# Kernel tuning notes

Hardware: AMD Instinct MI355X
Metric: run time of the kernel (lower is better)

The kernel has to match this reference:

```python
import jax, jax.numpy as jnp
import numpy as np

N = 40000      # nodes
E = 640000     # directed edges (avg degree 16)
IN_DIM = 64
HID = 64
OUT = 128
EPS_LN = 1e-5
EPS_BN = 1e-5
NEG_SLOPE = 0.2  # PyG GATConv default


def setup_inputs() -> dict:
    key = jax.random.key(0)
    ks = jax.random.split(key, 40)
    s = 0.05
    d = {}
    d["x"] = jax.random.normal(ks[0], (N, IN_DIM), jnp.float32)
    d["edge_index"] = jax.random.randint(ks[1], (2, E), 0, N, jnp.int32)
    d["pos"] = jax.random.normal(ks[2], (N, 3), jnp.float32)
    # GAT layer 1: in=64, out=64, heads=4 (concat)
    d["W1"] = jax.random.normal(ks[3], (4 * HID, IN_DIM), jnp.float32) * s
    d["a_s1"] = jax.random.normal(ks[4], (4, HID), jnp.float32) * s
    d["a_d1"] = jax.random.normal(ks[5], (4, HID), jnp.float32) * s
    d["bg1"] = jnp.zeros((4 * HID,), jnp.float32)
    d["ln1_g"] = jnp.ones((4 * HID,), jnp.float32)
    d["ln1_b"] = jnp.zeros((4 * HID,), jnp.float32)
    # GAT layer 2: in=256, out=64, heads=2 (concat)
    d["W2"] = jax.random.normal(ks[6], (2 * HID, 4 * HID), jnp.float32) * s
    d["a_s2"] = jax.random.normal(ks[7], (2, HID), jnp.float32) * s
    d["a_d2"] = jax.random.normal(ks[8], (2, HID), jnp.float32) * s
    d["bg2"] = jnp.zeros((2 * HID,), jnp.float32)
    d["ln2_g"] = jnp.ones((2 * HID,), jnp.float32)
    d["ln2_b"] = jnp.zeros((2 * HID,), jnp.float32)
    # GAT layer 3: in=128, out=128, heads=1
    d["W3"] = jax.random.normal(ks[9], (OUT, 2 * HID), jnp.float32) * s
    d["a_s3"] = jax.random.normal(ks[10], (1, OUT), jnp.float32) * s
    d["a_d3"] = jax.random.normal(ks[11], (1, OUT), jnp.float32) * s
    d["bg3"] = jnp.zeros((OUT,), jnp.float32)
    # pointnet: Conv1d(3,64,1) -> BN -> ReLU -> Conv1d(64,128,1) -> BN -> ReLU -> Conv1d(128,128,1)
    d["pw1"] = jax.random.normal(ks[12], (64, 3), jnp.float32) * s
    d["pb1"] = jnp.zeros((64,), jnp.float32)
    d["bn1_g"] = jnp.ones((64,), jnp.float32)
    d["bn1_b"] = jnp.zeros((64,), jnp.float32)
    d["pw2"] = jax.random.normal(ks[13], (128, 64), jnp.float32) * s
    d["pb2"] = jnp.zeros((128,), jnp.float32)
    d["bn2_g"] = jnp.ones((128,), jnp.float32)
    d["bn2_b"] = jnp.zeros((128,), jnp.float32)
    d["pw3"] = jax.random.normal(ks[14], (OUT, 128), jnp.float32) * s
    d["pb3"] = jnp.zeros((OUT,), jnp.float32)
    # fusion Linear(2*OUT, OUT)
    d["fw"] = jax.random.normal(ks[15], (OUT, 2 * OUT), jnp.float32) * s
    d["fb"] = jnp.zeros((OUT,), jnp.float32)
    return d


def _gat(x, W, a_s, a_d, b, src, dst, n):
    """PyG-style GATConv (concat=True, eval mode). x:[n,Fin], W:[H*C,Fin], a_*:[H,C]."""
    H, C = a_s.shape
    h = (x @ W.T).reshape(n, H, C)                       # [n,H,C]
    e_src = jnp.sum(h * a_s[None], -1)                   # [n,H]
    e_dst = jnp.sum(h * a_d[None], -1)                   # [n,H]
    e = jax.nn.leaky_relu(e_src[src] + e_dst[dst], NEG_SLOPE)   # [E,H]
    emax = jax.ops.segment_max(e, dst, num_segments=n)   # segment softmax over dst
    ex = jnp.exp(e - emax[dst])
    den = jax.ops.segment_sum(ex, dst, num_segments=n)
    alpha = ex / (den[dst] + 1e-16)                      # [E,H]
    out = jax.ops.segment_sum(alpha[:, :, None] * h[src], dst, num_segments=n)  # [n,H,C]
    return out.reshape(n, H * C) + b


def _ln(x, g, b):
    mu = jnp.mean(x, -1, keepdims=True)
    var = jnp.var(x, -1, keepdims=True)
    return (x - mu) * jax.lax.rsqrt(var + EPS_LN) * g + b


def _bn_eval(x, g, b):
    # eval-mode BatchNorm with freshly-initialized running stats (mean=0, var=1)
    return x * (g * jax.lax.rsqrt(jnp.float32(1.0 + EPS_BN))) + b


def reference(x, edge_index, pos, W1, a_s1, a_d1, bg1, ln1_g, ln1_b,
              W2, a_s2, a_d2, bg2, ln2_g, ln2_b, W3, a_s3, a_d3, bg3,
              pw1, pb1, bn1_g, bn1_b, pw2, pb2, bn2_g, bn2_b, pw3, pb3, fw, fb):
    n = x.shape[0]
    loops = jnp.arange(n, dtype=edge_index.dtype)        # PyG add_self_loops=True
    src = jnp.concatenate([edge_index[0], loops])
    dst = jnp.concatenate([edge_index[1], loops])

    x1 = jax.nn.relu(_ln(_gat(x, W1, a_s1, a_d1, bg1, src, dst, n), ln1_g, ln1_b))
    x2 = jax.nn.relu(_ln(_gat(x1, W2, a_s2, a_d2, bg2, src, dst, n), ln2_g, ln2_b))
    x3 = _gat(x2, W3, a_s3, a_d3, bg3, src, dst, n)      # [n,OUT]

    # pointnet: 1x1 conv1d == per-node linear
    p = jax.nn.relu(_bn_eval(pos @ pw1.T + pb1, bn1_g, bn1_b))
    p = jax.nn.relu(_bn_eval(p @ pw2.T + pb2, bn2_g, bn2_b))
    pos_features = p @ pw3.T + pb3                       # [n,OUT]

    combined = jnp.concatenate([x3, pos_features], -1)
    output = combined @ fw.T + fb
    return (output, x3, pos_features)
```

## Files before the change

kernel.cpp:

```cpp
#include <hip/hip_runtime.h>
#include <cstddef>

#define NNODES 40000
#define NEDGES 640000
#define NETOT  (NNODES + NEDGES)
#define ELLW   96
#define NCAST  30720
#define NBUCK  313
#define SEGCAP 8192
#define ABLOCKS 84
#define CBLOCKS 30
#define GBLK   625

typedef unsigned short u16;
typedef unsigned int   u32;
using v2f = __attribute__((ext_vector_type(2))) float;

__device__ inline float wave_sum(float v) {
#pragma unroll
    for (int o = 32; o > 0; o >>= 1) v += __shfl_xor(v, o);
    return v;
}
__device__ inline u16 f2bf(float f) {
    u32 u = __float_as_uint(f);
    return (u16)((u + 0x7fffu + ((u >> 16) & 1u)) >> 16);
}

__global__ void build_a_kernel(const int* __restrict__ ei, u32* __restrict__ bcnt,
                               u32* __restrict__ seg,
                               const float* __restrict__ W1, const float* __restrict__ as1,
                               const float* __restrict__ ad1, float* __restrict__ vbuf,
                               const float* s0, u16* d0, int n0, const float* s1, u16* d1, int n1,
                               const float* s2, u16* d2, int n2, const float* s3, u16* d3, int n3,
                               const float* s4, u16* d4, int n4, const float* s5, u16* d5, int n5) {
    int tid = threadIdx.x;
    int blk = blockIdx.x;
    if (blk >= ABLOCKS) {
        if (blk < ABLOCKS + CBLOCKS) {
            int i = (blk - ABLOCKS) * 1024 + tid;
            const float* s; u16* d;
            if      (i < n0) { s = s0; d = d0; }
            else if ((i -= n0) < n1) { s = s1; d = d1; }
            else if ((i -= n1) < n2) { s = s2; d = d2; }
            else if ((i -= n2) < n3) { s = s3; d = d3; }
            else if ((i -= n3) < n4) { s = s4; d = d4; }
            else if ((i -= n4) < n5) { s = s5; d = d5; }
            else return;
            float4 v = ((const float4*)s)[i];
            ushort4 o; o.x = f2bf(v.x); o.y = f2bf(v.y); o.z = f2bf(v.z); o.w = f2bf(v.w);
            ((ushort4*)d)[i] = o;
        } else if (tid < 256) {
            int h = tid >> 6, k = tid & 63;
            float ss = 0.f, dd = 0.f;
            for (int c = 0; c < 64; c++) {
                float w = W1[(h * 64 + c) * 64 + k];
                ss += as1[h * 64 + c] * w;
                dd += ad1[h * 64 + c] * w;
            }
            vbuf[tid] = ss;
            vbuf[256 + tid] = dd;
        }
        return;
    }
    __shared__ u32 hist[NBUCK], hbase[NBUCK];
    for (int i = tid; i < NBUCK; i += 1024) hist[i] = 0;
    __syncthreads();
    u32 pk[8], loc[8]; int bj[8];
    int g0 = blk * 8192;
#pragma unroll
    for (int j = 0; j < 8; j++) {
        int g = g0 + j * 1024 + tid;
        bj[j] = -1;
        if (g < NETOT) {
            int src, dst;
            if (g < NEDGES) { src = ei[g]; dst = ei[NEDGES + g]; }
            else            { src = g - NEDGES; dst = src; }
            int b = dst >> 7;
            pk[j] = ((u32)dst << 16) | (u32)src;
            bj[j] = b;
            loc[j] = atomicAdd(&hist[b], 1u);
        }
    }
    __syncthreads();
    for (int i = tid; i < NBUCK; i += 1024) {
        u32 c = hist[i];
        hbase[i] = c ? atomicAdd(&bcnt[i], c) : 0u;
    }
    __syncthreads();
#pragma unroll
    for (int j = 0; j < 8; j++) {
        if (bj[j] >= 0) {
            u32 pos = hbase[bj[j]] + loc[j];
            if (pos < SEGCAP) seg[(size_t)bj[j] * SEGCAP + pos] = pk[j];
        }
    }
}

__global__ void mid_kernel(const u32* __restrict__ seg, const u32* __restrict__ bcnt,
                           int* __restrict__ cnt, u16* __restrict__ srcs16,
                           int2* __restrict__ ovbuf,
                           const float* __restrict__ x, const float* __restrict__ vbuf,
                           float* __restrict__ es, float* __restrict__ ed, u16* __restrict__ xc,
                           const float* __restrict__ pos,
                           const float* __restrict__ pw1, const float* __restrict__ pb1,
                           const float* __restrict__ bn1g, const float* __restrict__ bn1b,
                           const u16* __restrict__ Bpn, u16* __restrict__ p2out,
                           const float* __restrict__ pb2,
                           const float* __restrict__ bn2g, const float* __restrict__ bn2b) {
    __shared__ u32 lcnt[128];
    __shared__ float vl[512];
    int tid = threadIdx.x;
    int blk = blockIdx.x;

    if (blk < NBUCK) {
        int base = blk << 7;
        if (tid < 128) lcnt[tid] = 0;
        __syncthreads();
        u32 m = bcnt[blk]; if (m > SEGCAP) m = SEGCAP;
        const u32* sp = seg + (size_t)blk * SEGCAP;
        for (u32 e = tid; e < m; e += 256) {
            u32 pkv = sp[e];
            u32 dst = pkv >> 16, src = pkv & 0xffffu;
            u32 p = atomicAdd(&lcnt[dst - (u32)base], 1u);
            if (p < ELLW) srcs16[dst * ELLW + p] = (u16)src;
            else {
                int q = atomicAdd(&cnt[NNODES], 1);
                ovbuf[q] = make_int2((int)dst, (int)src);
            }
        }
        __syncthreads();
        if (tid < 128 && base + tid < NNODES) cnt[base + tid] = (int)lcnt[tid];
        return;
    }
    blk -= NBUCK;
    if (blk < GBLK) {
        vl[tid] = vbuf[tid];
        vl[tid + 256] = vbuf[tid + 256];
        __syncthreads();
        int lane = tid & 63, wave = tid >> 6;
        int i = lane >> 2, q = lane & 3;
        int node = blk * 64 + wave * 16 + i;
        const float* xp = x + (size_t)node * 64 + q * 16;
        float xr[16];
        *(float4*)&xr[0]  = ((const float4*)xp)[0];
        *(float4*)&xr[4]  = ((const float4*)xp)[1];
        *(float4*)&xr[8]  = ((const float4*)xp)[2];
        *(float4*)&xr[12] = ((const float4*)xp)[3];
        float p[8];
#pragma unroll
        for (int h = 0; h < 8; h++) {
            float s = 0.f;
#pragma unroll
            for (int j = 0; j < 16; j++) s += xr[j] * vl[h * 64 + q * 16 + j];
            p[h] = s;
        }
#pragma unroll
        for (int h = 0; h < 8; h++) {
            p[h] += __shfl_xor(p[h], 1);
            p[h] += __shfl_xor(p[h], 2);
        }
        es[node * 4 + q] = p[q];
        ed[node * 4 + q] = p[4 + q];
        u16* cp = xc + (size_t)node * 64 + q * 16;
#pragma unroll
        for (int j = 0; j < 16; j += 4) {
            ushort4 o; o.x = f2bf(xr[j]); o.y = f2bf(xr[j + 1]);
            o.z = f2bf(xr[j + 2]); o.w = f2bf(xr[j + 3]);
            *(ushort4*)(cp + j) = o;
        }
        return;
    }
    blk -= GBLK;
    {
        const int Nn = 128, K = 64;
        using bfrag = __attribute__((ext_vector_type(8))) short;
        using ffrag = __attribute__((ext_vector_type(4))) float;
        int wave = tid >> 6, lane = tid & 63;
        int lm = lane & 15, kg = (lane >> 4) * 8;
        int rowblk = blk * 64 + wave * 16;
        int row = rowblk + lm;
        float p0 = pos[row * 3 + 0], p1 = pos[row * 3 + 1], p2 = pos[row * 3 + 2];
        const u16* Bp = Bpn + (size_t)lm * K + kg;
        const float bnscale = rsqrtf(1.0f + 1e-5f);
        ffrag acc[8] = {};
#pragma unroll
        for (int k0 = 0; k0 < K; k0 += 32) {
            bfrag af;
#pragma unroll
            for (int j = 0; j < 8; j++) {
                int k = kg + k0 + j;
                float v = p0 * pw1[k * 3 + 0] + p1 * pw1[k * 3 + 1] + p2 * pw1[k * 3 + 2] + pb1[k];
                v = v * (bn1g[k] * bnscale) + bn1b[k];
                v = v > 0.f ? v : 0.f;
                af[j] = (short)f2bf(v);
            }
#pragma unroll
            for (int t = 0; t < 8; t++) {
                bfrag bf = *(const bfrag*)(Bp + (size_t)t * 16 * K + k0);
                acc[t] = __builtin_amdgcn_mfma_f32_16x16x32_bf16(af, bf, acc[t], 0, 0, 0);
            }
        }
        int orow = rowblk + (lane >> 4) * 4;
#pragma unroll
        for (int t = 0; t < 8; t++) {
            int col = t * 16 + lm;
            float bi = pb2[col], g = bn2g[col] * bnscale, bb = bn2b[col];
#pragma unroll
            for (int r = 0; r < 4; r++) {
                float v = (acc[t][r] + bi) * g + bb;
                v = v > 0.f ? v : 0.f;
                p2out[(size_t)(orow + r) * Nn + col] = f2bf(v);
            }
        }
    }
}

__global__ void gat_agg_kernel(const u16* __restrict__ xc,
                               const float* __restrict__ es, const float* __restrict__ ed,
                               const int* __restrict__ cnt, const u16* __restrict__ srcs16,
                               const int2* __restrict__ ovbuf,
                               u16* __restrict__ agg, int n) {
    __shared__ float wbuf[4][4][100];
    __shared__ u32   sbuf[4][ELLW];
    int wave = threadIdx.x >> 6;
    int wid = (blockIdx.x * blockDim.x + threadIdx.x) >> 6;
    int lane = threadIdx.x & 63;
    if (wid >= n) return;

    int degt = cnt[wid];
    int mainc = degt < ELLW ? degt : ELLW;
    int padt = (mainc + 7) & ~7;
    const u16* sp = srcs16 + (size_t)wid * ELLW;

    const int h = lane & 3;
    const int esub = lane >> 2;
    float edh = ed[(size_t)wid * 4 + h];

    float den = 0.f;
    for (int i0 = 0; i0 < padt; i0 += 16) {
        int e = i0 + esub;
        if (e < padt) {
            float w = 0.f; u32 off = 0;
            if (e < mainc) {
                int s = sp[e];
                off = (u32)s << 7;
                float v = es[(size_t)s * 4 + h] + edh;
                v = v > 0.f ? v : 0.2f * v;
                w = __expf(v);
            }
            wbuf[wave][h][e] = w;
            if (h == 0) sbuf[wave][e] = off;
            den += w;
        }
    }
    int ovn = 0;
    if (degt > ELLW) {
        ovn = cnt[n];
        for (int j = esub; j < ovn; j += 16) {
            int2 t = ovbuf[j];
            if (t.x == wid) {
                float v = es[(size_t)t.y * 4 + h] + edh;
                v = v > 0.f ? v : 0.2f * v;
                den += __expf(v);
            }
        }
    }
#pragma unroll
    for (int o = 4; o < 64; o <<= 1) den += __shfl_xor(den, o);
    float inv = 1.f / (den + 1e-16f);

    const int e2 = lane >> 5, f16 = lane & 31;
    const char* hp = (const char*)xc + f16 * 4;
    v2f a0 = {0.f, 0.f}, a1 = {0.f, 0.f}, a2 = {0.f, 0.f}, a3 = {0.f, 0.f};
    for (int eb = 0; eb < padt; eb += 8) {
        u32 of[4]; u32 g[4];
        float w0[4], w1[4], w2[4], w3[4];
#pragma unroll
        for (int k = 0; k < 4; k++) of[k] = sbuf[wave][eb + 2 * k + e2];
#pragma unroll
        for (int k = 0; k < 4; k++) g[k] = *(const u32*)(hp + of[k]);
#pragma unroll
        for (int k = 0; k < 4; k++) {
            int e = eb + 2 * k + e2;
            w0[k] = wbuf[wave][0][e]; w1[k] = wbuf[wave][1][e];
            w2[k] = wbuf[wave][2][e]; w3[k] = wbuf[wave][3][e];
        }
#pragma unroll
        for (int k = 0; k < 4; k++) {
            v2f hx;
            hx.x = __uint_as_float(g[k] << 16);
            hx.y = __uint_as_float(g[k] & 0xffff0000u);
            a0 += v2f{w0[k], w0[k]} * hx;
            a1 += v2f{w1[k], w1[k]} * hx;
            a2 += v2f{w2[k], w2[k]} * hx;
            a3 += v2f{w3[k], w3[k]} * hx;
        }
    }
    if (degt > ELLW) {
        for (int j = 0; j < ovn; j++) {
            int2 t = ovbuf[j];
            if (t.x != wid) continue;
            float wh[4];
#pragma unroll
            for (int hh = 0; hh < 4; hh++) {
                float v = es[(size_t)t.y * 4 + hh] + __shfl(edh, hh);
                v = v > 0.f ? v : 0.2f * v;
                wh[hh] = __expf(v);
            }
            if (lane < 32) {
                u32 g = *(const u32*)(hp + ((u32)t.y << 7));
                v2f hx;
                hx.x = __uint_as_float(g << 16);
                hx.y = __uint_as_float(g & 0xffff0000u);
                a0 += v2f{wh[0], wh[0]} * hx;
                a1 += v2f{wh[1], wh[1]} * hx;
                a2 += v2f{wh[2], wh[2]} * hx;
                a3 += v2f{wh[3], wh[3]} * hx;
            }
        }
    }
    a0.x += __shfl_xor(a0.x, 32); a0.y += __shfl_xor(a0.y, 32);
    a1.x += __shfl_xor(a1.x, 32); a1.y += __shfl_xor(a1.y, 32);
    a2.x += __shfl_xor(a2.x, 32); a2.y += __shfl_xor(a2.y, 32);
    a3.x += __shfl_xor(a3.x, 32); a3.y += __shfl_xor(a3.y, 32);
    float iv[4];
#pragma unroll
    for (int hh = 0; hh < 4; hh++) iv[hh] = __shfl(inv, hh);
    if (lane < 32) {
        u32* op = (u32*)agg + (size_t)wid * 128 + f16;
        op[0]  = ((u32)f2bf(a0.y * iv[0]) << 16) | f2bf(a0.x * iv[0]);
        op[32] = ((u32)f2bf(a1.y * iv[1]) << 16) | f2bf(a1.x * iv[1]);
        op[64] = ((u32)f2bf(a2.y * iv[2]) << 16) | f2bf(a2.x * iv[2]);
        op[96] = ((u32)f2bf(a3.y * iv[3]) << 16) | f2bf(a3.x * iv[3]);
    }
}

__global__ __launch_bounds__(256, 2) void w1ln_kernel(
                            const u16* __restrict__ agg, const u16* __restrict__ B,
                            const float* __restrict__ bias,
                            const float* __restrict__ lng, const float* __restrict__ lnb,
                            u16* __restrict__ xb, int M) {
    using bfrag = __attribute__((ext_vector_type(8))) short;
    using ffrag = __attribute__((ext_vector_type(4))) float;
    int wave = threadIdx.x >> 6, lane = threadIdx.x & 63;
    int lm = lane & 15, kg = (lane >> 4) * 8;
    int rowblk = blockIdx.x * 64 + wave * 16;
    ffrag acc[16] = {};
#pragma unroll
    for (int hh = 0; hh < 4; hh++) {
#pragma unroll
        for (int k0 = 0; k0 < 64; k0 += 32) {
            bfrag af = *(const bfrag*)(agg + (size_t)(rowblk + lm) * 256 + hh * 64 + kg + k0);
            bfrag bfs[4];
#pragma unroll
            for (int tt = 0; tt < 4; tt++)
                bfs[tt] = *(const bfrag*)(B + (size_t)(hh * 64 + tt * 16 + lm) * 64 + kg + k0);
#pragma unroll
            for (int tt = 0; tt < 4; tt++) {
                int t = hh * 4 + tt;
                acc[t] = __builtin_amdgcn_mfma_f32_16x16x32_bf16(af, bfs[tt], acc[t], 0, 0, 0);
            }
        }
    }
    int orow = rowblk + (lane >> 4) * 4;
    float bi[16], gg[16], bb[16];
#pragma unroll
    for (int t = 0; t < 16; t++) {
        int col = t * 16 + lm;
        bi[t] = bias[col]; gg[t] = lng[col]; bb[t] = lnb[col];
    }
#pragma unroll
    for (int r = 0; r < 4; r++) {
        float pv[16];
        float s1 = 0.f, s2 = 0.f;
#pragma unroll
        for (int t = 0; t < 16; t++) {
            float v = acc[t][r] + bi[t];
            pv[t] = v; s1 += v; s2 += v * v;
        }
#pragma unroll
        for (int o = 1; o < 16; o <<= 1) { s1 += __shfl_xor(s1, o); s2 += __shfl_xor(s2, o); }
        float mu = s1 / 256.f;
        float var = s2 / 256.f - mu * mu;
        float rstd = rsqrtf(var + 1e-5f);
#pragma unroll
        for (int t = 0; t < 16; t++) {
            float v = (pv[t] - mu) * rstd * gg[t] + bb[t];
            v = v > 0.f ? v : 0.f;
            xb[(size_t)(orow + r) * 256 + t * 16 + lm] = f2bf(v);
        }
    }
}

template <int H, int C, bool AF32>
__global__ __launch_bounds__(256, 2) void gemm_scores_kernel(
                                   const void* __restrict__ Aptr, const u16* __restrict__ B,
                                   u16* __restrict__ Cout,
                                   const float* __restrict__ as, const float* __restrict__ ad,
                                   float* __restrict__ es, float* __restrict__ ed,
                                   int M, int Nn, int K) {
    constexpr int HT = 128 / C;
    using bfrag = __attribute__((ext_vector_type(8))) short;
    using ffrag = __attribute__((ext_vector_type(4))) float;
    int wave = threadIdx.x >> 6, lane = threadIdx.x & 63;
    int lm = lane & 15, kg = (lane >> 4) * 8;
    int rowblk = blockIdx.x * 64 + wave * 16;
    int n0 = blockIdx.y * 128;
    const u16* Bp = B + (size_t)(n0 + lm) * K + kg;
    ffrag acc[8] = {};
    for (int k0 = 0; k0 < K; k0 += 32) {
        bfrag af;
        if constexpr (AF32) {
            const float* ap = (const float*)Aptr + (size_t)(rowblk + lm) * K + kg + k0;
            float4 a0 = *(const float4*)ap;
            float4 a1 = *(const float4*)(ap + 4);
            af[0] = (short)f2bf(a0.x); af[1] = (short)f2bf(a0.y);
            af[2] = (short)f2bf(a0.z); af[3] = (short)f2bf(a0.w);
            af[4] = (short)f2bf(a1.x); af[5] = (short)f2bf(a1.y);
            af[6] = (short)f2bf(a1.z); af[7] = (short)f2bf(a1.w);
        } else {
            af = *(const bfrag*)((const u16*)Aptr + (size_t)(rowblk + lm) * K + kg + k0);
        }
        bfrag bfs[8];
#pragma unroll
        for (int t = 0; t < 8; t++)
            bfs[t] = *(const bfrag*)(Bp + (size_t)t * 16 * K + k0);
#pragma unroll
        for (int t = 0; t < 8; t++)
            acc[t] = __builtin_amdgcn_mfma_f32_16x16x32_bf16(af, bfs[t], acc[t], 0, 0, 0);
    }
    int orow = rowblk + (lane >> 4) * 4;
    float asv[8], adv[8];
#pragma unroll
    for (int t = 0; t < 8; t++) {
        int fcol = n0 + t * 16 + lm;
        asv[t] = as[fcol]; adv[t] = ad[fcol];
    }
    float ps[4][HT] = {}, pd[4][HT] = {};
#pragma unroll
    for (int t = 0; t < 8; t++) {
        const int hh = t / (C / 16);
#pragma unroll
        for (int r = 0; r < 4; r++) {
            float v = acc[t][r];
            ps[r][hh] += v * asv[t];
            pd[r][hh] += v * adv[t];
            Cout[(size_t)(orow + r) * Nn + n0 + t * 16 + lm] = f2bf(v);
        }
    }
    int hb = blockIdx.y * HT;
#pragma unroll
    for (int r = 0; r < 4; r++)
#pragma unroll
        for (int hh = 0; hh < HT; hh++) {
            float s = ps[r][hh], d = pd[r][hh];
#pragma unroll
            for (int o = 1; o < 16; o <<= 1) { s += __shfl_xor(s, o); d += __shfl_xor(d, o); }
            if (lm == 0) {
                es[(size_t)(orow + r) * H + hb + hh] = s;
                ed[(size_t)(orow + r) * H + hb + hh] = d;
            }
        }
}

template <int H, int C, bool LNRELU>
__global__ void gat_fused_kernel(const u16* __restrict__ hmat,
                                 const float* __restrict__ es, const float* __restrict__ ed,
                                 const int* __restrict__ cnt, const u16* __restrict__ srcs16,
                                 const int2* __restrict__ ovbuf,
                                 const float* __restrict__ bias,
                                 const float* __restrict__ lng, const float* __restrict__ lnb,
                                 void* __restrict__ out, u16* __restrict__ x16out, int n) {
    constexpr int HC = H * C;
    constexpr int VPT = HC / 64;
    constexpr int SH = (HC == 256) ? 9 : 8;
    constexpr int EPW = 64 / H;
    constexpr int HSH = (H == 4) ? 2 : ((H == 2) ? 1 : 0);
    __shared__ float wbuf[4][H][100];
    __shared__ int   sbuf[4][ELLW];
    int wave = threadIdx.x >> 6;
    int wid = (blockIdx.x * blockDim.x + threadIdx.x) >> 6;
    int lane = threadIdx.x & 63;
    if (wid >= n) return;

    int degt = cnt[wid];
    int mainc = degt < ELLW ? degt : ELLW;
    int pad = (mainc + 7) & ~7;
    const u16* sp = srcs16 + (size_t)wid * ELLW;

    const int h = lane & (H - 1);
    const int esub = lane >> HSH;
    float edh = ed[(size_t)wid * H + h];

    float den = 0.f;
    for (int i0 = 0; i0 < pad; i0 += EPW) {
        int e = i0 + esub;
        if (e < pad) {
            float w = 0.f;
            int soff = 0;
            if (e < mainc) {
                int s = sp[e];
                soff = s << SH;
                float v = es[(size_t)s * H + h] + edh;
                v = v > 0.f ? v : 0.2f * v;
                w = __expf(v);
            }
            wbuf[wave][h][e] = w;
            if (h == 0) sbuf[wave][e] = soff;
            den += w;
        }
    }
    int ovn = 0;
    if (degt > ELLW) {
        ovn = cnt[n];
        for (int j = esub; j < ovn; j += EPW) {
            int2 t = ovbuf[j];
            if (t.x == wid) {
                float v = es[(size_t)t.y * H + h] + edh;
                v = v > 0.f ? v : 0.2f * v;
                den += __expf(v);
            }
        }
    }
#pragma unroll
    for (int o = H; o < 64; o <<= 1) den += __shfl_xor(den, o);
    float inv = 1.f / (den + 1e-16f);

    const int myhead = (lane * VPT) / C;
    const float invh = __shfl(inv, myhead);
    const int loff = lane * (VPT * 2);
    v2f a01 = {0.f, 0.f}, a23 = {0.f, 0.f};

    for (int e = 0; e < pad; e += 8) {
        int4   o0 = *(const int4*)&sbuf[wave][e];
        int4   o1 = *(const int4*)&sbuf[wave][e + 4];
        float4 w0 = *(const float4*)&wbuf[wave][myhead][e];
        float4 w1 = *(const float4*)&wbuf[wave][myhead][e + 4];
        int   oo[8] = {o0.x, o0.y, o0.z, o0.w, o1.x, o1.y, o1.z, o1.w};
        float ww[8] = {w0.x, w0.y, w0.z, w0.w, w1.x, w1.y, w1.z, w1.w};
        if constexpr (VPT == 4) {
            uint2 gg[8];
#pragma unroll
            for (int u = 0; u < 8; u++)
                gg[u] = *(const uint2*)((const char*)hmat + (size_t)(u32)oo[u] + loff);
#pragma unroll
            for (int u = 0; u < 8; u++) {
                v2f wv = {ww[u], ww[u]};
                v2f h01, h23;
                h01.x = __uint_as_float(gg[u].x << 16);
                h01.y = __uint_as_float(gg[u].x & 0xffff0000u);
                h23.x = __uint_as_float(gg[u].y << 16);
                h23.y = __uint_as_float(gg[u].y & 0xffff0000u);
                a01 += wv * h01;
                a23 += wv * h23;
            }
        } else {
            u32 gg[8];
#pragma unroll
            for (int u = 0; u < 8; u++)
                gg[u] = *(const u32*)((const char*)hmat + (size_t)(u32)oo[u] + loff);
#pragma unroll
            for (int u = 0; u < 8; u++) {
                v2f wv = {ww[u], ww[u]};
                v2f h01;
                h01.x = __uint_as_float(gg[u] << 16);
                h01.y = __uint_as_float(gg[u] & 0xffff0000u);
                a01 += wv * h01;
            }
        }
    }
    if (degt > ELLW) {
        const float edm = __shfl(edh, myhead);
        for (int j = 0; j < ovn; j++) {
            int2 t = ovbuf[j];
            if (t.x != wid) continue;
            float v = es[(size_t)t.y * H + myhead] + edm;
            v = v > 0.f ? v : 0.2f * v;
            float w = __expf(v);
            v2f wv = {w, w};
            if constexpr (VPT == 4) {
                uint2 g = *(const uint2*)((const char*)hmat + ((size_t)t.y << SH) + loff);
                v2f h01, h23;
                h01.x = __uint_as_float(g.x << 16);
                h01.y = __uint_as_float(g.x & 0xffff0000u);
                h23.x = __uint_as_float(g.y << 16);
                h23.y = __uint_as_float(g.y & 0xffff0000u);
                a01 += wv * h01;
                a23 += wv * h23;
            } else {
                u32 g = *(const u32*)((const char*)hmat + ((size_t)t.y << SH) + loff);
                v2f h01;
                h01.x = __uint_as_float(g << 16);
                h01.y = __uint_as_float(g & 0xffff0000u);
                a01 += wv * h01;
            }
        }
    }
    {
        v2f iv = {invh, invh};
        a01 *= iv;
        a23 *= iv;
    }

    int fbase = lane * VPT;
    float y[VPT];
    y[0] = a01.x + bias[fbase + 0];
    y[1] = a01.y + bias[fbase + 1];
    if constexpr (VPT == 4) {
        y[2] = a23.x + bias[fbase + 2];
        y[3] = a23.y + bias[fbase + 3];
    }

    if constexpr (LNRELU) {
        float s1 = 0.f, s2 = 0.f;
#pragma unroll
        for (int j = 0; j < VPT; j++) { s1 += y[j]; s2 += y[j] * y[j]; }
        s1 = wave_sum(s1);
        s2 = wave_sum(s2);
        float mu = s1 / (float)HC;
        float var = s2 / (float)HC - mu * mu;
        float rstd = rsqrtf(var + 1e-5f);
#pragma unroll
        for (int j = 0; j < VPT; j++) {
            float v = (y[j] - mu) * rstd * lng[fbase + j] + lnb[fbase + j];
            y[j] = v > 0.f ? v : 0.f;
        }
        u16* op = (u16*)out + (size_t)wid * HC + fbase;
        if constexpr (VPT == 4) {
            ushort4 o; o.x = f2bf(y[0]); o.y = f2bf(y[1]); o.z = f2bf(y[2]); o.w = f2bf(y[3]);
            *(ushort4*)op = o;
        } else {
            ushort2 o; o.x = f2bf(y[0]); o.y = f2bf(y[1]);
            *(ushort2*)op = o;
        }
    } else {
        float* op = (float*)out + (size_t)wid * HC + fbase;
        if constexpr (VPT == 4) *(float4*)op = make_float4(y[0], y[1], y[2], y[3]);
        else                    *(float2*)op = make_float2(y[0], y[1]);
        if (x16out) {
            if constexpr (VPT == 4) {
                ushort4 o; o.x = f2bf(y[0]); o.y = f2bf(y[1]); o.z = f2bf(y[2]); o.w = f2bf(y[3]);
                *(ushort4*)&x16out[(size_t)wid * HC + fbase] = o;
            } else {
                ushort2 o; o.x = f2bf(y[0]); o.y = f2bf(y[1]);
                *(ushort2*)&x16out[(size_t)wid * HC + fbase] = o;
            }
        }
    }
}

__global__ void pf_kernel(const u16* __restrict__ p2, const u16* __restrict__ Bpw3,
                          const float* __restrict__ pb3, float* __restrict__ pf,
                          u16* __restrict__ pfb, int M) {
    using bfrag = __attribute__((ext_vector_type(8))) short;
    using ffrag = __attribute__((ext_vector_type(4))) float;
    __shared__ u16 bl[128][136];
    int tid = threadIdx.x;
    for (int i = tid; i < 2048; i += 256) {
        int r = i >> 4, c = (i & 15) * 8;
        *(uint4*)&bl[r][c] = *(const uint4*)(Bpw3 + (size_t)r * 128 + c);
    }
    __syncthreads();
    int wave = tid >> 6, lane = tid & 63;
    int lm = lane & 15, kg = (lane >> 4) * 8;
    int row = blockIdx.x * 64 + wave * 16 + lm;
    bfrag afs[4];
#pragma unroll
    for (int i = 0; i < 4; i++)
        afs[i] = *(const bfrag*)(p2 + (size_t)row * 128 + kg + i * 32);
    ffrag acc[8] = {};
#pragma unroll
    for (int k = 0; k < 4; k++)
#pragma unroll
        for (int t = 0; t < 8; t++) {
            bfrag bf = *(const bfrag*)&bl[t * 16 + lm][kg + k * 32];
            acc[t] = __builtin_amdgcn_mfma_f32_16x16x32_bf16(afs[k], bf, acc[t], 0, 0, 0);
        }
    int orow = blockIdx.x * 64 + wave * 16 + (lane >> 4) * 4;
#pragma unroll
    for (int t = 0; t < 8; t++) {
        int col = t * 16 + lm;
        float bi = pb3[col];
#pragma unroll
        for (int r = 0; r < 4; r++) {
            float v = acc[t][r] + bi;
            pf[(size_t)(orow + r) * 128 + col] = v;
            pfb[(size_t)(orow + r) * 128 + col] = f2bf(v);
        }
    }
}

__global__ void out_kernel(const u16* __restrict__ x3b, const u16* __restrict__ pfb,
                           const u16* __restrict__ Bfw, const float* __restrict__ fb,
                           float* __restrict__ outp, int M) {
    using bfrag = __attribute__((ext_vector_type(8))) short;
    using ffrag = __attribute__((ext_vector_type(4))) float;
    __shared__ u16 bl[128][264];
    int tid = threadIdx.x;
    for (int i = tid; i < 4096; i += 256) {
        int r = i >> 5, c = (i & 31) * 8;
        *(uint4*)&bl[r][c] = *(const uint4*)(Bfw + (size_t)r * 256 + c);
    }
    __syncthreads();
    int wave = tid >> 6, lane = tid & 63;
    int lm = lane & 15, kg = (lane >> 4) * 8;
    int row = blockIdx.x * 64 + wave * 16 + lm;
    bfrag afs[8];
#pragma unroll
    for (int i = 0; i < 4; i++)
        afs[i] = *(const bfrag*)(x3b + (size_t)row * 128 + kg + i * 32);
#pragma unroll
    for (int i = 0; i < 4; i++)
        afs[4 + i] = *(const bfrag*)(pfb + (size_t)row * 128 + kg + i * 32);
    ffrag acc[8] = {};
#pragma unroll
    for (int k = 0; k < 8; k++)
#pragma unroll
        for (int t = 0; t < 8; t++) {
            bfrag bf = *(const bfrag*)&bl[t * 16 + lm][kg + k * 32];
            acc[t] = __builtin_amdgcn_mfma_f32_16x16x32_bf16(afs[k], bf, acc[t], 0, 0, 0);
        }
    int orow = blockIdx.x * 64 + wave * 16 + (lane >> 4) * 4;
#pragma unroll
    for (int t = 0; t < 8; t++) {
        int col = t * 16 + lm;
        float bi = fb[col];
#pragma unroll
        for (int r = 0; r < 4; r++)
            outp[(size_t)(orow + r) * 128 + col] = acc[t][r] + bi;
    }
}

extern "C" void kernel_launch(void* const* d_in, const int* in_sizes, int n_in,
                              void* d_out, int out_size, void* d_ws, size_t ws_size,
                              hipStream_t stream) {
    const float* x    = (const float*)d_in[0];
    const int*   ei   = (const int*)d_in[1];
    const float* pos  = (const float*)d_in[2];
    const float* W1   = (const float*)d_in[3];
    const float* as1  = (const float*)d_in[4];
    const float* ad1  = (const float*)d_in[5];
    const float* bg1  = (const float*)d_in[6];
    const float* ln1g = (const float*)d_in[7];
    const float* ln1b = (const float*)d_in[8];
    const float* W2   = (const float*)d_in[9];
    const float* as2  = (const float*)d_in[10];
    const float* ad2  = (const float*)d_in[11];
    const float* bg2  = (const float*)d_in[12];
    const float* ln2g = (const float*)d_in[13];
    const float* ln2b = (const float*)d_in[14];
    const float* W3   = (const float*)d_in[15];
    const float* as3  = (const float*)d_in[16];
    const float* ad3  = (const float*)d_in[17];
    const float* bg3  = (const float*)d_in[18];
    const float* pw1  = (const float*)d_in[19];
    const float* pb1  = (const float*)d_in[20];
    const float* bn1g = (const float*)d_in[21];
    const float* bn1b = (const float*)d_in[22];
    const float* pw2  = (const float*)d_in[23];
    const float* pb2  = (const float*)d_in[24];
    const float* bn2g = (const float*)d_in[25];
    const float* bn2b = (const float*)d_in[26];
    const float* pw3  = (const float*)d_in[27];
    const float* pb3  = (const float*)d_in[28];
    const float* fw   = (const float*)d_in[29];
    const float* fb   = (const float*)d_in[30];

    const int N = NNODES;
    float* out = (float*)d_out;
    float* x3  = out + (size_t)N * 128;
    float* pf  = out + (size_t)2 * N * 128;

    char* ws = (char*)d_ws;
    size_t off = 0;
    auto alloc = [&](size_t bytes) -> void* {
        void* p = ws + off;
        off += (bytes + 255) / 256 * 256;
        return p;
    };
    int*   cnt    = (int*)alloc((size_t)(N + 1 + NBUCK) * 4);
    u32*   bcnt   = (u32*)(cnt + N + 1);
    u32*   seg    = (u32*)alloc((size_t)NBUCK * SEGCAP * 4);
    u16*   srcs16 = (u16*)alloc((size_t)N * ELLW * 2);
    int2*  ovbuf  = (int2*)alloc((size_t)NETOT * 8);
    float* esb    = (float*)alloc((size_t)N * 4 * 4);
    float* edb    = (float*)alloc((size_t)N * 4 * 4);
    u16*   w1c    = (u16*)alloc(16384 * 2);
    u16*   w2c    = (u16*)alloc(32768 * 2);
    u16*   w3c    = (u16*)alloc(16384 * 2);
    u16*   pw2c   = (u16*)alloc(8192 * 2);
    u16*   pw3c   = (u16*)alloc(16384 * 2);
    u16*   fwc    = (u16*)alloc(32768 * 2);
    u16*   hbufb  = (u16*)alloc((size_t)N * 128 * 2);
    u16*   xb     = (u16*)alloc((size_t)N * 256 * 2);
    u16*   p2b    = (u16*)alloc((size_t)N * 128 * 2);
    u16*   xc     = (u16*)alloc((size_t)N * 64 * 2);
    float* vbuf   = (float*)alloc(512 * 4);
    u16*   aggb   = (u16*)alloc((size_t)N * 256 * 2);
    u16*   x3b    = (u16*)alloc((size_t)N * 128 * 2);
    u16*   pfb    = (u16*)alloc((size_t)N * 128 * 2);

    hipMemsetAsync(cnt, 0, (size_t)(N + 1 + NBUCK) * 4, stream);
    build_a_kernel<<<ABLOCKS + CBLOCKS + 1, 1024, 0, stream>>>(
        ei, bcnt, seg, W1, as1, ad1, vbuf,
        W1, w1c, 4096, W2, w2c, 8192, W3, w3c, 4096,
        pw2, pw2c, 2048, pw3, pw3c, 4096, fw, fwc, 8192);

    mid_kernel<<<NBUCK + 2 * GBLK, 256, 0, stream>>>(
        seg, bcnt, cnt, srcs16, ovbuf,
        x, vbuf, esb, edb, xc,
        pos, pw1, pb1, bn1g, bn1b, pw2c, p2b, pb2, bn2g, bn2b);

    const int NW = N / 4;
    const int GB = GBLK;

    gat_agg_kernel<<<NW, 256, 0, stream>>>(xc, esb, edb, cnt, srcs16, ovbuf, aggb, N);
    w1ln_kernel<<<GB, 256, 0, stream>>>(aggb, w1c, bg1, ln1g, ln1b, xb, N);

    gemm_scores_kernel<2, 64, false><<<dim3(GB, 1), 256, 0, stream>>>(
        xb, w2c, hbufb, as2, ad2, esb, edb, N, 128, 256);
    gat_fused_kernel<2, 64, true><<<NW, 256, 0, stream>>>(
        hbufb, esb, edb, cnt, srcs16, ovbuf, bg2, ln2g, ln2b, xb, nullptr, N);

    gemm_scores_kernel<1, 128, false><<<dim3(GB, 1), 256, 0, stream>>>(
        xb, w3c, hbufb, as3, ad3, esb, edb, N, 128, 128);
    gat_fused_kernel<1, 128, false><<<NW, 256, 0, stream>>>(
        hbufb, esb, edb, cnt, srcs16, ovbuf, bg3, nullptr, nullptr, x3, x3b, N);

    pf_kernel<<<GB, 256, 0, stream>>>(p2b, pw3c, pb3, pf, pfb, N);
    out_kernel<<<GB, 256, 0, stream>>>(x3b, pfb, fwc, fb, out, N);
}
```

Before: 334.8 us.

## Aggregate before W3 projection and fold W3 into fusion weights

```diff
diff --git a/kernel.cpp b/kernel.cpp
--- a/kernel.cpp
+++ b/kernel.cpp
@@ -5,11 +5,11 @@
 #define NEDGES 640000
 #define NETOT  (NNODES + NEDGES)
 #define ELLW   96
-#define NCAST  30720
 #define NBUCK  313
 #define SEGCAP 8192
 #define ABLOCKS 84
 #define CBLOCKS 30
+#define ACB (ABLOCKS + CBLOCKS)
 #define GBLK   625
 
 typedef unsigned short u16;
@@ -30,13 +30,18 @@
                                u32* __restrict__ seg,
                                const float* __restrict__ W1, const float* __restrict__ as1,
                                const float* __restrict__ ad1, float* __restrict__ vbuf,
+                               const float* __restrict__ W3, const float* __restrict__ as3,
+                               const float* __restrict__ ad3, float* __restrict__ v3buf,
+                               const float* __restrict__ fwf, const float* __restrict__ bg3,
+                               const float* __restrict__ fbf,
+                               u16* __restrict__ bcomb, float* __restrict__ cvec,
                                const float* s0, u16* d0, int n0, const float* s1, u16* d1, int n1,
                                const float* s2, u16* d2, int n2, const float* s3, u16* d3, int n3,
                                const float* s4, u16* d4, int n4, const float* s5, u16* d5, int n5) {
     int tid = threadIdx.x;
     int blk = blockIdx.x;
     if (blk >= ABLOCKS) {
-        if (blk < ABLOCKS + CBLOCKS) {
+        if (blk < ACB) {
             int i = (blk - ABLOCKS) * 1024 + tid;
             const float* s; u16* d;
             if      (i < n0) { s = s0; d = d0; }
@@ -49,16 +54,45 @@
             float4 v = ((const float4*)s)[i];
             ushort4 o; o.x = f2bf(v.x); o.y = f2bf(v.y); o.z = f2bf(v.z); o.w = f2bf(v.w);
             ((ushort4*)d)[i] = o;
-        } else if (tid < 256) {
-            int h = tid >> 6, k = tid & 63;
-            float ss = 0.f, dd = 0.f;
-            for (int c = 0; c < 64; c++) {
-                float w = W1[(h * 64 + c) * 64 + k];
-                ss += as1[h * 64 + c] * w;
-                dd += ad1[h * 64 + c] * w;
-            }
-            vbuf[tid] = ss;
-            vbuf[256 + tid] = dd;
+        } else if (blk == ACB) {
+            if (tid < 256) {
+                int h = tid >> 6, k = tid & 63;
+                float ss = 0.f, dd = 0.f;
+                for (int c = 0; c < 64; c++) {
+                    float w = W1[(h * 64 + c) * 64 + k];
+                    ss += as1[h * 64 + c] * w;
+                    dd += ad1[h * 64 + c] * w;
+                }
+                vbuf[tid] = ss;
+                vbuf[256 + tid] = dd;
+            }
+        } else if (blk == ACB + 1) {
+            if (tid < 128) {
+                float ss = 0.f, dd = 0.f;
+                for (int c = 0; c < 128; c++) {
+                    float w = W3[c * 128 + tid];
+                    ss += as3[c] * w;
+                    dd += ad3[c] * w;
+                }
+                v3buf[tid] = ss;
+                v3buf[128 + tid] = dd;
+            }
+        } else if (blk < ACB + 2 + 32) {
+            int e = (blk - (ACB + 2)) * 1024 + tid;
+            int o = e >> 8, d = e & 255;
+            if (d < 128) {
+                float s = 0.f;
+                for (int k = 0; k < 128; k++) s += fwf[o * 256 + k] * W3[k * 128 + d];
+                bcomb[o * 256 + d] = f2bf(s);
+            } else {
+                bcomb[o * 256 + d] = f2bf(fwf[o * 256 + d]);
+            }
+        } else {
+            if (tid < 128) {
+                float s = fbf[tid];
+                for (int k = 0; k < 128; k++) s += fwf[tid * 256 + k] * bg3[k];
+                cvec[tid] = s;
+            }
         }
         return;
     }
@@ -392,75 +426,97 @@
     }
 }
 
-template <int H, int C, bool AF32>
-__global__ __launch_bounds__(256, 2) void gemm_scores_kernel(
-                                   const void* __restrict__ Aptr, const u16* __restrict__ B,
-                                   u16* __restrict__ Cout,
-                                   const float* __restrict__ as, const float* __restrict__ ad,
-                                   float* __restrict__ es, float* __restrict__ ed,
-                                   int M, int Nn, int K) {
-    constexpr int HT = 128 / C;
+__global__ __launch_bounds__(256, 2) void gs2pf_kernel(
+        const u16* __restrict__ xb, const u16* __restrict__ B2, u16* __restrict__ Cout,
+        const float* __restrict__ as2, const float* __restrict__ ad2,
+        float* __restrict__ es, float* __restrict__ ed,
+        const u16* __restrict__ p2, const u16* __restrict__ Bpw3,
+        const float* __restrict__ pb3, float* __restrict__ pf, u16* __restrict__ pfb, int M) {
     using bfrag = __attribute__((ext_vector_type(8))) short;
     using ffrag = __attribute__((ext_vector_type(4))) float;
-    int wave = threadIdx.x >> 6, lane = threadIdx.x & 63;
+    __shared__ u16 bl[128][136];
+    int tid = threadIdx.x;
+    int blk = blockIdx.x;
+    int wave = tid >> 6, lane = tid & 63;
     int lm = lane & 15, kg = (lane >> 4) * 8;
-    int rowblk = blockIdx.x * 64 + wave * 16;
-    int n0 = blockIdx.y * 128;
-    const u16* Bp = B + (size_t)(n0 + lm) * K + kg;
-    ffrag acc[8] = {};
-    for (int k0 = 0; k0 < K; k0 += 32) {
-        bfrag af;
-        if constexpr (AF32) {
-            const float* ap = (const float*)Aptr + (size_t)(rowblk + lm) * K + kg + k0;
-            float4 a0 = *(const float4*)ap;
-            float4 a1 = *(const float4*)(ap + 4);
-            af[0] = (short)f2bf(a0.x); af[1] = (short)f2bf(a0.y);
-            af[2] = (short)f2bf(a0.z); af[3] = (short)f2bf(a0.w);
-            af[4] = (short)f2bf(a1.x); af[5] = (short)f2bf(a1.y);
-            af[6] = (short)f2bf(a1.z); af[7] = (short)f2bf(a1.w);
-        } else {
-            af = *(const bfrag*)((const u16*)Aptr + (size_t)(rowblk + lm) * K + kg + k0);
-        }
-        bfrag bfs[8];
-#pragma unroll
-        for (int t = 0; t < 8; t++)
-            bfs[t] = *(const bfrag*)(Bp + (size_t)t * 16 * K + k0);
-#pragma unroll
-        for (int t = 0; t < 8; t++)
-            acc[t] = __builtin_amdgcn_mfma_f32_16x16x32_bf16(af, bfs[t], acc[t], 0, 0, 0);
-    }
-    int orow = rowblk + (lane >> 4) * 4;
-    float asv[8], adv[8];
-#pragma unroll
-    for (int t = 0; t < 8; t++) {
-        int fcol = n0 + t * 16 + lm;
-        asv[t] = as[fcol]; adv[t] = ad[fcol];
-    }
-    float ps[4][HT] = {}, pd[4][HT] = {};
-#pragma unroll
-    for (int t = 0; t < 8; t++) {
-        const int hh = t / (C / 16);
-#pragma unroll
-        for (int r = 0; r < 4; r++) {
-            float v = acc[t][r];
-            ps[r][hh] += v * asv[t];
-            pd[r][hh] += v * adv[t];
-            Cout[(size_t)(orow + r) * Nn + n0 + t * 16 + lm] = f2bf(v);
-        }
-    }
-    int hb = blockIdx.y * HT;
-#pragma unroll
-    for (int r = 0; r < 4; r++)
-#pragma unroll
-        for (int hh = 0; hh < HT; hh++) {
-            float s = ps[r][hh], d = pd[r][hh];
-#pragma unroll
-            for (int o = 1; o < 16; o <<= 1) { s += __shfl_xor(s, o); d += __shfl_xor(d, o); }
-            if (lm == 0) {
-                es[(size_t)(orow + r) * H + hb + hh] = s;
-                ed[(size_t)(orow + r) * H + hb + hh] = d;
-            }
-        }
+    if (blk < GBLK) {
+        int rowblk = blk * 64 + wave * 16;
+        const u16* Bp = B2 + (size_t)lm * 256 + kg;
+        ffrag acc[8] = {};
+        for (int k0 = 0; k0 < 256; k0 += 32) {
+            bfrag af = *(const bfrag*)(xb + (size_t)(rowblk + lm) * 256 + kg + k0);
+            bfrag bfs[8];
+#pragma unroll
+            for (int t = 0; t < 8; t++)
+                bfs[t] = *(const bfrag*)(Bp + (size_t)t * 16 * 256 + k0);
+#pragma unroll
+            for (int t = 0; t < 8; t++)
+                acc[t] = __builtin_amdgcn_mfma_f32_16x16x32_bf16(af, bfs[t], acc[t], 0, 0, 0);
+        }
+        int orow = rowblk + (lane >> 4) * 4;
+        float asv[8], adv[8];
+#pragma unroll
+        for (int t = 0; t < 8; t++) {
+            int fcol = t * 16 + lm;
+            asv[t] = as2[fcol]; adv[t] = ad2[fcol];
+        }
+        float ps[4][2] = {}, pd[4][2] = {};
+#pragma unroll
+        for (int t = 0; t < 8; t++) {
+            const int hh = t >> 2;
+#pragma unroll
+            for (int r = 0; r < 4; r++) {
+                float v = acc[t][r];
+                ps[r][hh] += v * asv[t];
+                pd[r][hh] += v * adv[t];
+                Cout[(size_t)(orow + r) * 128 + t * 16 + lm] = f2bf(v);
+            }
+        }
+#pragma unroll
+        for (int r = 0; r < 4; r++)
+#pragma unroll
+            for (int hh = 0; hh < 2; hh++) {
+                float s = ps[r][hh], d = pd[r][hh];
+#pragma unroll
+                for (int o = 1; o < 16; o <<= 1) { s += __shfl_xor(s, o); d += __shfl_xor(d, o); }
+                if (lm == 0) {
+                    es[(size_t)(orow + r) * 2 + hh] = s;
+                    ed[(size_t)(orow + r) * 2 + hh] = d;
+                }
+            }
+    } else {
+        blk -= GBLK;
+        for (int i = tid; i < 2048; i += 256) {
+            int r = i >> 4, c = (i & 15) * 8;
+            *(uint4*)&bl[r][c] = *(const uint4*)(Bpw3 + (size_t)r * 128 + c);
+        }
+        __syncthreads();
+        int row = blk * 64 + wave * 16 + lm;
+        bfrag afs[4];
+#pragma unroll
+        for (int i = 0; i < 4; i++)
+            afs[i] = *(const bfrag*)(p2 + (size_t)row * 128 + kg + i * 32);
+        ffrag acc[8] = {};
+#pragma unroll
+        for (int k = 0; k < 4; k++)
+#pragma unroll
+            for (int t = 0; t < 8; t++) {
+                bfrag bf = *(const bfrag*)&bl[t * 16 + lm][kg + k * 32];
+                acc[t] = __builtin_amdgcn_mfma_f32_16x16x32_bf16(afs[k], bf, acc[t], 0, 0, 0);
+            }
+        int orow = blk * 64 + wave * 16 + (lane >> 4) * 4;
+#pragma unroll
+        for (int t = 0; t < 8; t++) {
+            int col = t * 16 + lm;
+            float bi = pb3[col];
+#pragma unroll
+            for (int r = 0; r < 4; r++) {
+                float v = acc[t][r] + bi;
+                pf[(size_t)(orow + r) * 128 + col] = v;
+                pfb[(size_t)(orow + r) * 128 + col] = f2bf(v);
+            }
+        }
+    }
 }
 
 template <int H, int C, bool LNRELU>
@@ -470,7 +526,9 @@
                                  const int2* __restrict__ ovbuf,
                                  const float* __restrict__ bias,
                                  const float* __restrict__ lng, const float* __restrict__ lnb,
-                                 void* __restrict__ out, u16* __restrict__ x16out, int n) {
+                                 void* __restrict__ out, u16* __restrict__ x16out,
+                                 const float* __restrict__ v3, const float* __restrict__ v3d,
+                                 float* __restrict__ es3o, float* __restrict__ ed3o, int n) {
     constexpr int HC = H * C;
     constexpr int VPT = HC / 64;
     constexpr int SH = (HC == 256) ? 9 : 8;
@@ -604,11 +662,12 @@
 
     int fbase = lane * VPT;
     float y[VPT];
-    y[0] = a01.x + bias[fbase + 0];
-    y[1] = a01.y + bias[fbase + 1];
-    if constexpr (VPT == 4) {
-        y[2] = a23.x + bias[fbase + 2];
-        y[3] = a23.y + bias[fbase + 3];
+    y[0] = a01.x;
+    y[1] = a01.y;
+    if constexpr (VPT == 4) { y[2] = a23.x; y[3] = a23.y; }
+    if (bias) {
+#pragma unroll
+        for (int j = 0; j < VPT; j++) y[j] += bias[fbase + j];
     }
 
     if constexpr (LNRELU) {
@@ -624,6 +683,17 @@
         for (int j = 0; j < VPT; j++) {
             float v = (y[j] - mu) * rstd * lng[fbase + j] + lnb[fbase + j];
             y[j] = v > 0.f ? v : 0.f;
+        }
+        if (v3) {
+            float s3 = 0.f, d3 = 0.f;
+#pragma unroll
+            for (int j = 0; j < VPT; j++) {
+                s3 += y[j] * v3[fbase + j];
+                d3 += y[j] * v3d[fbase + j];
+            }
+            s3 = wave_sum(s3);
+            d3 = wave_sum(d3);
+            if (lane == 0) { es3o[wid] = s3; ed3o[wid] = d3; }
         }
         u16* op = (u16*)out + (size_t)wid * HC + fbase;
         if constexpr (VPT == 4) {
@@ -634,9 +704,11 @@
             *(ushort2*)op = o;
         }
     } else {
-        float* op = (float*)out + (size_t)wid * HC + fbase;
-        if constexpr (VPT == 4) *(float4*)op = make_float4(y[0], y[1], y[2], y[3]);
-        else                    *(float2*)op = make_float2(y[0], y[1]);
+        if (out) {
+            float* op = (float*)out + (size_t)wid * HC + fbase;
+            if constexpr (VPT == 4) *(float4*)op = make_float4(y[0], y[1], y[2], y[3]);
+            else                    *(float2*)op = make_float2(y[0], y[1]);
+        }
         if (x16out) {
             if constexpr (VPT == 4) {
                 ushort4 o; o.x = f2bf(y[0]); o.y = f2bf(y[1]); o.z = f2bf(y[2]); o.w = f2bf(y[3]);
@@ -649,85 +721,77 @@
     }
 }
 
-__global__ void pf_kernel(const u16* __restrict__ p2, const u16* __restrict__ Bpw3,
-                          const float* __restrict__ pb3, float* __restrict__ pf,
-                          u16* __restrict__ pfb, int M) {
-    using bfrag = __attribute__((ext_vector_type(8))) short;
-    using ffrag = __attribute__((ext_vector_type(4))) float;
-    __shared__ u16 bl[128][136];
-    int tid = threadIdx.x;
-    for (int i = tid; i < 2048; i += 256) {
-        int r = i >> 4, c = (i & 15) * 8;
-        *(uint4*)&bl[r][c] = *(const uint4*)(Bpw3 + (size_t)r * 128 + c);
-    }
-    __syncthreads();
-    int wave = tid >> 6, lane = tid & 63;
-    int lm = lane & 15, kg = (lane >> 4) * 8;
-    int row = blockIdx.x * 64 + wave * 16 + lm;
-    bfrag afs[4];
-#pragma unroll
-    for (int i = 0; i < 4; i++)
-        afs[i] = *(const bfrag*)(p2 + (size_t)row * 128 + kg + i * 32);
-    ffrag acc[8] = {};
-#pragma unroll
-    for (int k = 0; k < 4; k++)
-#pragma unroll
-        for (int t = 0; t < 8; t++) {
-            bfrag bf = *(const bfrag*)&bl[t * 16 + lm][kg + k * 32];
-            acc[t] = __builtin_amdgcn_mfma_f32_16x16x32_bf16(afs[k], bf, acc[t], 0, 0, 0);
-        }
-    int orow = blockIdx.x * 64 + wave * 16 + (lane >> 4) * 4;
-#pragma unroll
-    for (int t = 0; t < 8; t++) {
-        int col = t * 16 + lm;
-        float bi = pb3[col];
-#pragma unroll
-        for (int r = 0; r < 4; r++) {
-            float v = acc[t][r] + bi;
-            pf[(size_t)(orow + r) * 128 + col] = v;
-            pfb[(size_t)(orow + r) * 128 + col] = f2bf(v);
-        }
-    }
-}
-
-__global__ void out_kernel(const u16* __restrict__ x3b, const u16* __restrict__ pfb,
-                           const u16* __restrict__ Bfw, const float* __restrict__ fb,
-                           float* __restrict__ outp, int M) {
+__global__ void w3out_kernel(const u16* __restrict__ agg3b, const u16* __restrict__ w3c,
+                             const float* __restrict__ bg3, float* __restrict__ x3,
+                             const u16* __restrict__ pfb, const u16* __restrict__ bcomb,
+                             const float* __restrict__ cvec, float* __restrict__ outp, int M) {
     using bfrag = __attribute__((ext_vector_type(8))) short;
     using ffrag = __attribute__((ext_vector_type(4))) float;
     __shared__ u16 bl[128][264];
     int tid = threadIdx.x;
-    for (int i = tid; i < 4096; i += 256) {
-        int r = i >> 5, c = (i & 31) * 8;
-        *(uint4*)&bl[r][c] = *(const uint4*)(Bfw + (size_t)r * 256 + c);
-    }
-    __syncthreads();
+    int blk = blockIdx.x;
     int wave = tid >> 6, lane = tid & 63;
     int lm = lane & 15, kg = (lane >> 4) * 8;
-    int row = blockIdx.x * 64 + wave * 16 + lm;
-    bfrag afs[8];
-#pragma unroll
-    for (int i = 0; i < 4; i++)
-        afs[i] = *(const bfrag*)(x3b + (size_t)row * 128 + kg + i * 32);
-#pragma unroll
-    for (int i = 0; i < 4; i++)
-        afs[4 + i] = *(const bfrag*)(pfb + (size_t)row * 128 + kg + i * 32);
-    ffrag acc[8] = {};
-#pragma unroll
-    for (int k = 0; k < 8; k++)
+    if (blk < GBLK) {
+        for (int i = tid; i < 2048; i += 256) {
+            int r = i >> 4, c = (i & 15) * 8;
+            *(uint4*)&bl[r][c] = *(const uint4*)(w3c + (size_t)r * 128 + c);
+        }
+        __syncthreads();
+        int row = blk * 64 + wave * 16 + lm;
+        bfrag afs[4];
+#pragma unroll
+        for (int i = 0; i < 4; i++)
+            afs[i] = *(const bfrag*)(agg3b + (size_t)row * 128 + kg + i * 32);
+        ffrag acc[8] = {};
+#pragma unroll
+        for (int k = 0; k < 4; k++)
+#pragma unroll
+            for (int t = 0; t < 8; t++) {
+                bfrag bf = *(const bfrag*)&bl[t * 16 + lm][kg + k * 32];
+                acc[t] = __builtin_amdgcn_mfma_f32_16x16x32_bf16(afs[k], bf, acc[t], 0, 0, 0);
+            }
+        int orow = blk * 64 + wave * 16 + (lane >> 4) * 4;
 #pragma unroll
         for (int t = 0; t < 8; t++) {
-            bfrag bf = *(const bfrag*)&bl[t * 16 + lm][kg + k * 32];
-            acc[t] = __builtin_amdgcn_mfma_f32_16x16x32_bf16(afs[k], bf, acc[t], 0, 0, 0);
-        }
-    int orow = blockIdx.x * 64 + wave * 16 + (lane >> 4) * 4;
-#pragma unroll
-    for (int t = 0; t < 8; t++) {
-        int col = t * 16 + lm;
-        float bi = fb[col];
-#pragma unroll
-        for (int r = 0; r < 4; r++)
-            outp[(size_t)(orow + r) * 128 + col] = acc[t][r] + bi;
+            int col = t * 16 + lm;
+            float bi = bg3[col];
+#pragma unroll
+            for (int r = 0; r < 4; r++)
+                x3[(size_t)(orow + r) * 128 + col] = acc[t][r] + bi;
+        }
+    } else {
+        blk -= GBLK;
+        for (int i = tid; i < 4096; i += 256) {
+            int r = i >> 5, c = (i & 31) * 8;
+            *(uint4*)&bl[r][c] = *(const uint4*)(bcomb + (size_t)r * 256 + c);
+        }
+        __syncthreads();
+        int row = blk * 64 + wave * 16 + lm;
+        bfrag afs[8];
+#pragma unroll
+        for (int i = 0; i < 4; i++)
+            afs[i] = *(const bfrag*)(agg3b + (size_t)row * 128 + kg + i * 32);
+#pragma unroll
+        for (int i = 0; i < 4; i++)
+            afs[4 + i] = *(const bfrag*)(pfb + (size_t)row * 128 + kg + i * 32);
+        ffrag acc[8] = {};
+#pragma unroll
+        for (int k = 0; k < 8; k++)
+#pragma unroll
+            for (int t = 0; t < 8; t++) {
+                bfrag bf = *(const bfrag*)&bl[t * 16 + lm][kg + k * 32];
+                acc[t] = __builtin_amdgcn_mfma_f32_16x16x32_bf16(afs[k], bf, acc[t], 0, 0, 0);
+            }
+        int orow = blk * 64 + wave * 16 + (lane >> 4) * 4;
+#pragma unroll
+        for (int t = 0; t < 8; t++) {
+            int col = t * 16 + lm;
+            float bi = cvec[col];
+#pragma unroll
+            for (int r = 0; r < 4; r++)
+                outp[(size_t)(orow + r) * 128 + col] = acc[t][r] + bi;
+        }
     }
 }
 
@@ -785,24 +849,30 @@
     int2*  ovbuf  = (int2*)alloc((size_t)NETOT * 8);
     float* esb    = (float*)alloc((size_t)N * 4 * 4);
     float* edb    = (float*)alloc((size_t)N * 4 * 4);
+    float* es3b   = (float*)alloc((size_t)N * 4);
+    float* ed3b   = (float*)alloc((size_t)N * 4);
     u16*   w1c    = (u16*)alloc(16384 * 2);
     u16*   w2c    = (u16*)alloc(32768 * 2);
     u16*   w3c    = (u16*)alloc(16384 * 2);
     u16*   pw2c   = (u16*)alloc(8192 * 2);
     u16*   pw3c   = (u16*)alloc(16384 * 2);
     u16*   fwc    = (u16*)alloc(32768 * 2);
+    u16*   bcomb  = (u16*)alloc(32768 * 2);
+    float* cvec   = (float*)alloc(128 * 4);
     u16*   hbufb  = (u16*)alloc((size_t)N * 128 * 2);
     u16*   xb     = (u16*)alloc((size_t)N * 256 * 2);
     u16*   p2b    = (u16*)alloc((size_t)N * 128 * 2);
     u16*   xc     = (u16*)alloc((size_t)N * 64 * 2);
     float* vbuf   = (float*)alloc(512 * 4);
+    float* v3buf  = (float*)alloc(256 * 4);
     u16*   aggb   = (u16*)alloc((size_t)N * 256 * 2);
-    u16*   x3b    = (u16*)alloc((size_t)N * 128 * 2);
+    u16*   agg3b  = (u16*)alloc((size_t)N * 128 * 2);
     u16*   pfb    = (u16*)alloc((size_t)N * 128 * 2);
 
     hipMemsetAsync(cnt, 0, (size_t)(N + 1 + NBUCK) * 4, stream);
-    build_a_kernel<<<ABLOCKS + CBLOCKS + 1, 1024, 0, stream>>>(
-        ei, bcnt, seg, W1, as1, ad1, vbuf,
+    build_a_kernel<<<ACB + 35, 1024, 0, stream>>>(
+        ei, bcnt, seg, W1, as1, ad1, vbuf, W3, as3, ad3, v3buf,
+        fw, bg3, fb, bcomb, cvec,
         W1, w1c, 4096, W2, w2c, 8192, W3, w3c, 4096,
         pw2, pw2c, 2048, pw3, pw3c, 4096, fw, fwc, 8192);
 
@@ -817,16 +887,17 @@
     gat_agg_kernel<<<NW, 256, 0, stream>>>(xc, esb, edb, cnt, srcs16, ovbuf, aggb, N);
     w1ln_kernel<<<GB, 256, 0, stream>>>(aggb, w1c, bg1, ln1g, ln1b, xb, N);
 
-    gemm_scores_kernel<2, 64, false><<<dim3(GB, 1), 256, 0, stream>>>(
-        xb, w2c, hbufb, as2, ad2, esb, edb, N, 128, 256);
+    gs2pf_kernel<<<2 * GB, 256, 0, stream>>>(
+        xb, w2c, hbufb, as2, ad2, esb, edb,
+        p2b, pw3c, pb3, pf, pfb, N);
+
     gat_fused_kernel<2, 64, true><<<NW, 256, 0, stream>>>(
-        hbufb, esb, edb, cnt, srcs16, ovbuf, bg2, ln2g, ln2b, xb, nullptr, N);
-
-    gemm_scores_kernel<1, 128, false><<<dim3(GB, 1), 256, 0, stream>>>(
-        xb, w3c, hbufb, as3, ad3, esb, edb, N, 128, 128);
+        hbufb, esb, edb, cnt, srcs16, ovbuf, bg2, ln2g, ln2b, xb, nullptr,
+        v3buf, v3buf + 128, es3b, ed3b, N);
+
     gat_fused_kernel<1, 128, false><<<NW, 256, 0, stream>>>(
-        hbufb, esb, edb, cnt, srcs16, ovbuf, bg3, nullptr, nullptr, x3, x3b, N);
-
-    pf_kernel<<<GB, 256, 0, stream>>>(p2b, pw3c, pb3, pf, pfb, N);
-    out_kernel<<<GB, 256, 0, stream>>>(x3b, pfb, fwc, fb, out, N);
+        xb, es3b, ed3b, cnt, srcs16, ovbuf, nullptr, nullptr, nullptr,
+        nullptr, agg3b, nullptr, nullptr, nullptr, nullptr, N);
+
+    w3out_kernel<<<2 * GB, 256, 0, stream>>>(agg3b, w3c, bg3, x3, pfb, bcomb, cvec, out, N);
 }
```

Result: faster. 309.9 us (-7.4%).
